# Optimization experiments

Measured on AMD Instinct MI355X. Metric: run time of the kernel, lower is better.

The kernel has to match this reference:

```python
import jax, jax.numpy as jnp
import numpy as np

N = 100000
E = 500000
F_IN = 128
HID = 64
HEADS = 4
OUT = 32
NEG_SLOPE = 0.2


def _glorot(key, shape):
    fan_in, fan_out = shape[0], shape[1]
    lim = jnp.sqrt(6.0 / (fan_in + fan_out))
    return jax.random.uniform(key, shape, jnp.float32, -lim, lim)


def setup_inputs() -> dict:
    key = jax.random.key(0)
    ks = jax.random.split(key, 20)
    x = jax.random.normal(ks[0], (N, F_IN), jnp.float32)
    edge_index = jax.random.randint(ks[1], (2, E), 0, N, jnp.int64)
    edge_attr = jax.random.uniform(ks[2], (E, 1), jnp.float32)
    d1 = HEADS * HID
    params = {
        # conv1: F_IN -> HEADS x HID
        "Wl1": _glorot(ks[3], (F_IN, d1)), "bl1": jnp.zeros((d1,), jnp.float32),
        "Wr1": _glorot(ks[4], (F_IN, d1)), "br1": jnp.zeros((d1,), jnp.float32),
        "We1": _glorot(ks[5], (1, d1)),
        "att1": _glorot(ks[6], (HEADS, HID)),
        "b1": jnp.zeros((d1,), jnp.float32),
        "Wl2": _glorot(ks[7], (d1, OUT)), "bl2": jnp.zeros((OUT,), jnp.float32),
        "Wr2": _glorot(ks[8], (d1, OUT)), "br2": jnp.zeros((OUT,), jnp.float32),
        "We2": _glorot(ks[9], (1, OUT)),
        "att2": _glorot(ks[10], (1, OUT)),
        "b2": jnp.zeros((OUT,), jnp.float32),
    }
    return {"x": x, "edge_index": edge_index, "edge_attr": edge_attr, **params}


def gatv2_conv(x, src, dst, edge_attr, Wl, bl, Wr, br, We, att, bias, heads, out_ch):
    """PyG GATv2Conv (add_self_loops=False, concat=True, share_weights=False)."""
    n = x.shape[0]
    xl = (x @ Wl + bl).reshape(n, heads, out_ch)          # source transform
    xr = (x @ Wr + br).reshape(n, heads, out_ch)          # target transform
    e = (edge_attr @ We).reshape(-1, heads, out_ch)       # [E, H, C]
    m = jax.nn.leaky_relu(xl[src] + xr[dst] + e, NEG_SLOPE)  # [E, H, C]
    alpha = jnp.einsum('ehc,hc->eh', m, att)              # [E, H]
    # softmax over edges sharing the same destination node
    amax = jax.ops.segment_max(alpha, dst, num_segments=n)
    ealpha = jnp.exp(alpha - amax[dst])
    denom = jax.ops.segment_sum(ealpha, dst, num_segments=n)
    alpha = ealpha / (denom[dst] + 1e-16)
    out = jax.ops.segment_sum(xl[src] * alpha[:, :, None], dst, num_segments=n)
    return out.reshape(n, heads * out_ch) + bias


def reference(x, edge_index, edge_attr, Wl1, bl1, Wr1, br1, We1, att1, b1,
              Wl2, bl2, Wr2, br2, We2, att2, b2):
    src, dst = edge_index[0], edge_index[1]
    h = gatv2_conv(x, src, dst, edge_attr, Wl1, bl1, Wr1, br1, We1, att1, b1, HEADS, HID)
    h = jax.nn.relu(h)  # dropout is identity at inference
    out = gatv2_conv(h, src, dst, edge_attr, Wl2, bl2, Wr2, br2, We2, att2, b2, 1, OUT)
    return out
```

## Files before the change

kernel.cpp:

```cpp
#include <hip/hip_runtime.h>
#include <cstddef>
#include <cstdint>

#define F_IN 128
#define D1   256
#define HEADS 4
#define HID   64
#define OUT_C 32
#define NEG   0.2f

typedef unsigned short ushort_t;
typedef __attribute__((ext_vector_type(8))) short short8;
typedef __attribute__((ext_vector_type(4))) float f32x4;
typedef __attribute__((ext_vector_type(4))) unsigned short ushort4v;

__device__ __forceinline__ float bu2f(ushort_t u) {
  return __uint_as_float(((unsigned)u) << 16);
}
__device__ __forceinline__ ushort_t f2bu(float f) {
  unsigned u = __float_as_uint(f);
  return (ushort_t)((u + 0x7FFF + ((u >> 16) & 1)) >> 16);
}

__global__ void prep_b1_k(const float* __restrict__ Wl, const float* __restrict__ Wr,
                          const float* __restrict__ bl, const float* __restrict__ br,
                          ushort_t* __restrict__ Bt, float* __restrict__ biasc) {
  int i = blockIdx.x * blockDim.x + threadIdx.x;
  int nn = i >> 7, k = i & 127;
  float v = (nn < D1) ? Wl[(size_t)k * D1 + nn] : Wr[(size_t)k * D1 + (nn - D1)];
  Bt[(size_t)nn * F_IN + k] = f2bu(v);
  if (k == 0) biasc[nn] = (nn < D1) ? bl[nn] : br[nn - D1];
}

__global__ void prep_b2_k(const float* __restrict__ Wl, const float* __restrict__ Wr,
                          const float* __restrict__ bl, const float* __restrict__ br,
                          ushort_t* __restrict__ Bt, float* __restrict__ biasc) {
  int i = blockIdx.x * blockDim.x + threadIdx.x;
  int nn = i >> 8, k = i & 255;
  float v = (nn < OUT_C) ? Wl[(size_t)k * OUT_C + nn] : Wr[(size_t)k * OUT_C + (nn - OUT_C)];
  Bt[(size_t)nn * D1 + k] = f2bu(v);
  if (k == 0) biasc[nn] = (nn < OUT_C) ? bl[nn] : br[nn - OUT_C];
}

template <int WM, int WN, int BK, bool CVT>
__global__ void mfma_gemm(const void* __restrict__ Av, const ushort_t* __restrict__ Bt,
                          const float* __restrict__ biasc, ushort_t* __restrict__ C,
                          int M, int N, int K) {
  constexpr int BM = WM * 64, BN = WN * 64;
  constexpr int LD = BK + 8;
  constexpr int CPR = BK / 8;
  __shared__ ushort_t As[BM][LD];
  __shared__ ushort_t Bs[BN][LD];
  const int tid = threadIdx.x;
  const int wave = tid >> 6, lane = tid & 63;
  const int wm = wave % WM, wn = wave / WM;
  const int quad = lane >> 4, l16 = lane & 15;
  const int m0 = blockIdx.x * BM, n0 = blockIdx.y * BN;
  const int nth = WM * WN * 64;
  f32x4 acc[4][4] = {};
  for (int k0 = 0; k0 < K; k0 += BK) {
    for (int i = tid; i < BM * CPR; i += nth) {
      int r = i / CPR, ch = i % CPR;
      int gr = m0 + r;
      if (CVT) {
        const float* A32 = (const float*)Av;
        f32x4 v0 = {}, v1 = {};
        if (gr < M) {
          const float* p = A32 + (size_t)gr * K + k0 + ch * 8;
          v0 = *(const f32x4*)p;
          v1 = *(const f32x4*)(p + 4);
        }
        short8 o;
        o[0] = (short)f2bu(v0[0]); o[1] = (short)f2bu(v0[1]);
        o[2] = (short)f2bu(v0[2]); o[3] = (short)f2bu(v0[3]);
        o[4] = (short)f2bu(v1[0]); o[5] = (short)f2bu(v1[1]);
        o[6] = (short)f2bu(v1[2]); o[7] = (short)f2bu(v1[3]);
        *(short8*)(&As[r][ch * 8]) = o;
      } else {
        const ushort_t* A16 = (const ushort_t*)Av;
        short8 v = {};
        if (gr < M) v = *(const short8*)(A16 + (size_t)gr * K + k0 + ch * 8);
        *(short8*)(&As[r][ch * 8]) = v;
      }
    }
    for (int i = tid; i < BN * CPR; i += nth) {
      int r = i / CPR, ch = i % CPR;
      short8 v = {};
      if (n0 + r < N) v = *(const short8*)(Bt + (size_t)(n0 + r) * K + k0 + ch * 8);
      *(short8*)(&Bs[r][ch * 8]) = v;
    }
    __syncthreads();
#pragma unroll
    for (int ks = 0; ks < BK; ks += 32) {
      short8 af[4], bfr[4];
#pragma unroll
      for (int mi = 0; mi < 4; ++mi)
        af[mi] = *(const short8*)(&As[wm * 64 + mi * 16 + l16][ks + quad * 8]);
#pragma unroll
      for (int ni = 0; ni < 4; ++ni)
        bfr[ni] = *(const short8*)(&Bs[wn * 64 + ni * 16 + l16][ks + quad * 8]);
#pragma unroll
      for (int mi = 0; mi < 4; ++mi)
#pragma unroll
        for (int ni = 0; ni < 4; ++ni)
          acc[mi][ni] = __builtin_amdgcn_mfma_f32_16x16x32_bf16(af[mi], bfr[ni],
                                                                acc[mi][ni], 0, 0, 0);
    }
    __syncthreads();
  }
#pragma unroll
  for (int mi = 0; mi < 4; ++mi) {
#pragma unroll
    for (int r = 0; r < 4; ++r) {
      int grow = m0 + wm * 64 + mi * 16 + quad * 4 + r;
      if (grow >= M) continue;
#pragma unroll
      for (int ni = 0; ni < 4; ++ni) {
        int gcol = n0 + wn * 64 + ni * 16 + l16;
        C[(size_t)grow * N + gcol] = f2bu(acc[mi][ni][r] + biasc[gcol]);
      }
    }
  }
}

__global__ void hist_k(const int* __restrict__ dst, int* __restrict__ deg, int e) {
  int i = blockIdx.x * blockDim.x + threadIdx.x;
  if (i < e) atomicAdd(&deg[dst[i]], 1);
}

__global__ void scan_block_k(const int* __restrict__ deg, int* __restrict__ row_ptr,
                             int* __restrict__ bsum, int n) {
  __shared__ int s[1024];
  int i = blockIdx.x * 1024 + threadIdx.x;
  int v = (i < n) ? deg[i] : 0;
  s[threadIdx.x] = v;
  __syncthreads();
  for (int off = 1; off < 1024; off <<= 1) {
    int t = (threadIdx.x >= off) ? s[threadIdx.x - off] : 0;
    __syncthreads();
    s[threadIdx.x] += t;
    __syncthreads();
  }
  if (i < n) row_ptr[i + 1] = s[threadIdx.x];
  if (threadIdx.x == 1023) bsum[blockIdx.x] = s[1023];
}

__global__ void scan_bsum_k(int* __restrict__ bsum, int nb) {
  __shared__ int s[128];
  int v = (threadIdx.x < nb) ? bsum[threadIdx.x] : 0;
  s[threadIdx.x] = v;
  __syncthreads();
  for (int off = 1; off < 128; off <<= 1) {
    int t = (threadIdx.x >= off) ? s[threadIdx.x - off] : 0;
    __syncthreads();
    s[threadIdx.x] += t;
    __syncthreads();
  }
  if (threadIdx.x < nb) bsum[threadIdx.x] = s[threadIdx.x] - v;
}

__global__ void add_off_k(int* __restrict__ row_ptr, const int* __restrict__ bsum, int n) {
  int i = blockIdx.x * blockDim.x + threadIdx.x;
  if (i == 0) row_ptr[0] = 0;
  if (i < n) row_ptr[i + 1] += bsum[i >> 10];
}

__global__ void copy_cursor_k(const int* __restrict__ row_ptr, int* __restrict__ cursor, int n) {
  int i = blockIdx.x * blockDim.x + threadIdx.x;
  if (i < n) cursor[i] = row_ptr[i];
}

__global__ void fill_k(const int* __restrict__ src, const int* __restrict__ dst,
                       const float* __restrict__ eattr, int* __restrict__ cursor,
                       int2* __restrict__ csr, int e) {
  int i = blockIdx.x * blockDim.x + threadIdx.x;
  if (i >= e) return;
  int p = atomicAdd(&cursor[dst[i]], 1);
  csr[p] = make_int2(src[i], __float_as_int(eattr[i]));
}

__global__ void gat1_k(const int* __restrict__ row_ptr, const int2* __restrict__ csr,
                       const ushort_t* __restrict__ C1,
                       const float* __restrict__ We, const float* __restrict__ att,
                       const float* __restrict__ bias, ushort_t* __restrict__ h1, int n) {
  int node = (int)(((size_t)blockIdx.x * blockDim.x + threadIdx.x) >> 6);
  int lane = threadIdx.x & 63;
  if (node >= n) return;
  int cb = lane * 4;
  ushort4v xr4 = *(const ushort4v*)(C1 + (size_t)node * 512 + 256 + cb);
  float xrr[4], Wev[4], attv[4], acc[4] = {0.f, 0.f, 0.f, 0.f};
  float esum = 0.f;
#pragma unroll
  for (int j = 0; j < 4; ++j) {
    xrr[j] = bu2f(xr4[j]);
    Wev[j] = We[cb + j];
    attv[j] = att[cb + j];
  }
  int p = row_ptr[node], p1 = row_ptr[node + 1];
  for (; p + 4 <= p1; p += 4) {
    int2 ee[4];
#pragma unroll
    for (int u = 0; u < 4; ++u) ee[u] = csr[p + u];
    ushort4v xl4[4];
#pragma unroll
    for (int u = 0; u < 4; ++u)
      xl4[u] = *(const ushort4v*)(C1 + (size_t)ee[u].x * 512 + cb);
    float xv[4][4], v[4];
#pragma unroll
    for (int u = 0; u < 4; ++u) {
      float wgt = __int_as_float(ee[u].y);
      v[u] = 0.f;
#pragma unroll
      for (int j = 0; j < 4; ++j) {
        xv[u][j] = bu2f(xl4[u][j]);
        float m = xv[u][j] + xrr[j] + wgt * Wev[j];
        m = m > 0.f ? m : NEG * m;
        v[u] += m * attv[j];
      }
    }
#pragma unroll
    for (int u = 0; u < 4; ++u) {
      v[u] += __shfl_xor(v[u], 1, 64);
      v[u] += __shfl_xor(v[u], 2, 64);
      v[u] += __shfl_xor(v[u], 4, 64);
      v[u] += __shfl_xor(v[u], 8, 64);
    }
#pragma unroll
    for (int u = 0; u < 4; ++u) {
      float eh = __expf(v[u]);
      esum += eh;
#pragma unroll
      for (int j = 0; j < 4; ++j) acc[j] += eh * xv[u][j];
    }
  }
  for (; p < p1; ++p) {
    int2 ed = csr[p];
    float wgt = __int_as_float(ed.y);
    ushort4v xl4 = *(const ushort4v*)(C1 + (size_t)ed.x * 512 + cb);
    float xv[4], v = 0.f;
#pragma unroll
    for (int j = 0; j < 4; ++j) {
      xv[j] = bu2f(xl4[j]);
      float m = xv[j] + xrr[j] + wgt * Wev[j];
      m = m > 0.f ? m : NEG * m;
      v += m * attv[j];
    }
    v += __shfl_xor(v, 1, 64);
    v += __shfl_xor(v, 2, 64);
    v += __shfl_xor(v, 4, 64);
    v += __shfl_xor(v, 8, 64);
    float eh = __expf(v);
    esum += eh;
#pragma unroll
    for (int j = 0; j < 4; ++j) acc[j] += eh * xv[j];
  }
  float inv = 1.f / (esum + 1e-16f);
  ushort4v o;
#pragma unroll
  for (int j = 0; j < 4; ++j) {
    float t = acc[j] * inv + bias[cb + j];
    o[j] = f2bu(t > 0.f ? t : 0.f);
  }
  *(ushort4v*)(h1 + (size_t)node * D1 + cb) = o;
}

__global__ void gat2_k(const int* __restrict__ row_ptr, const int2* __restrict__ csr,
                       const ushort_t* __restrict__ C2,
                       const float* __restrict__ We, const float* __restrict__ att,
                       const float* __restrict__ bias, float* __restrict__ out, int n) {
  size_t t = (size_t)blockIdx.x * blockDim.x + threadIdx.x;
  int node = (int)(t >> 3);
  int g = (int)(t & 7);
  if (node >= n) return;
  int cb = g * 4;
  ushort4v xr4 = *(const ushort4v*)(C2 + (size_t)node * 64 + 32 + cb);
  float xrr[4], Wev[4], attv[4], acc[4] = {0.f, 0.f, 0.f, 0.f};
  float esum = 0.f;
#pragma unroll
  for (int j = 0; j < 4; ++j) {
    xrr[j] = bu2f(xr4[j]);
    Wev[j] = We[cb + j];
    attv[j] = att[cb + j];
  }
  int p = row_ptr[node], p1 = row_ptr[node + 1];
  for (; p + 4 <= p1; p += 4) {
    int2 ee[4];
#pragma unroll
    for (int u = 0; u < 4; ++u) ee[u] = csr[p + u];
    ushort4v xl4[4];
#pragma unroll
    for (int u = 0; u < 4; ++u)
      xl4[u] = *(const ushort4v*)(C2 + (size_t)ee[u].x * 64 + cb);
    float xv[4][4], v[4];
#pragma unroll
    for (int u = 0; u < 4; ++u) {
      float wgt = __int_as_float(ee[u].y);
      v[u] = 0.f;
#pragma unroll
      for (int j = 0; j < 4; ++j) {
        xv[u][j] = bu2f(xl4[u][j]);
        float m = xv[u][j] + xrr[j] + wgt * Wev[j];
        m = m > 0.f ? m : NEG * m;
        v[u] += m * attv[j];
      }
    }
#pragma unroll
    for (int u = 0; u < 4; ++u) {
      v[u] += __shfl_xor(v[u], 1, 64);
      v[u] += __shfl_xor(v[u], 2, 64);
      v[u] += __shfl_xor(v[u], 4, 64);
    }
#pragma unroll
    for (int u = 0; u < 4; ++u) {
      float eh = __expf(v[u]);
      esum += eh;
#pragma unroll
      for (int j = 0; j < 4; ++j) acc[j] += eh * xv[u][j];
    }
  }
  for (; p < p1; ++p) {
    int2 ed = csr[p];
    float wgt = __int_as_float(ed.y);
    ushort4v xl4 = *(const ushort4v*)(C2 + (size_t)ed.x * 64 + cb);
    float xv[4], v = 0.f;
#pragma unroll
    for (int j = 0; j < 4; ++j) {
      xv[j] = bu2f(xl4[j]);
      float m = xv[j] + xrr[j] + wgt * Wev[j];
      m = m > 0.f ? m : NEG * m;
      v += m * attv[j];
    }
    v += __shfl_xor(v, 1, 64);
    v += __shfl_xor(v, 2, 64);
    v += __shfl_xor(v, 4, 64);
    float eh = __expf(v);
    esum += eh;
#pragma unroll
    for (int j = 0; j < 4; ++j) acc[j] += eh * xv[j];
  }
  float inv = 1.f / (esum + 1e-16f);
  f32x4 ov;
#pragma unroll
  for (int j = 0; j < 4; ++j) ov[j] = acc[j] * inv + bias[cb + j];
  *(f32x4*)(out + (size_t)node * OUT_C + cb) = ov;
}

extern "C" void kernel_launch(void* const* d_in, const int* in_sizes, int n_in,
                              void* d_out, int out_size, void* d_ws, size_t ws_size,
                              hipStream_t stream) {
  const float* x     = (const float*)d_in[0];
  const int*   eidx  = (const int*)d_in[1];
  const float* eattr = (const float*)d_in[2];
  const float* Wl1 = (const float*)d_in[3];
  const float* bl1 = (const float*)d_in[4];
  const float* Wr1 = (const float*)d_in[5];
  const float* br1 = (const float*)d_in[6];
  const float* We1 = (const float*)d_in[7];
  const float* att1 = (const float*)d_in[8];
  const float* b1  = (const float*)d_in[9];
  const float* Wl2 = (const float*)d_in[10];
  const float* bl2 = (const float*)d_in[11];
  const float* Wr2 = (const float*)d_in[12];
  const float* br2 = (const float*)d_in[13];
  const float* We2 = (const float*)d_in[14];
  const float* att2 = (const float*)d_in[15];
  const float* b2  = (const float*)d_in[16];

  const int n = in_sizes[0] / F_IN;
  const int e = in_sizes[2];
  const int* src = eidx;
  const int* dst = eidx + e;
  float* out = (float*)d_out;

  char* w = (char*)d_ws;
  ushort_t* C1   = (ushort_t*)w;  w += (size_t)n * 512 * 2;
  ushort_t* h1b  = (ushort_t*)w;  w += (size_t)n * D1 * 2;
  ushort_t* C2   = (ushort_t*)w;  w += (size_t)n * 64 * 2;
  ushort_t* Bt1  = (ushort_t*)w;  w += 512 * F_IN * 2;
  ushort_t* Bt2  = (ushort_t*)w;  w += 64 * D1 * 2;
  float* bias1c  = (float*)w;     w += 512 * 4;
  float* bias2c  = (float*)w;     w += 64 * 4;
  int2*  csr     = (int2*)w;      w += (size_t)e * 8;
  int*   row_ptr = (int*)w;       w += ((size_t)n + 1) * 4;
  int*   cursor  = (int*)w;       w += (size_t)n * 4;
  int*   bsum    = (int*)w;       w += 512;
  int*   deg = cursor;

  dim3 blk(256);
  const int nb = (n + 1023) / 1024;

  prep_b1_k<<<(512 * 128) / 256, blk, 0, stream>>>(Wl1, Wr1, bl1, br1, Bt1, bias1c);
  prep_b2_k<<<(64 * 256) / 256, blk, 0, stream>>>(Wl2, Wr2, bl2, br2, Bt2, bias2c);

  hipMemsetAsync(deg, 0, (size_t)n * sizeof(int), stream);
  hist_k<<<(e + 255) / 256, blk, 0, stream>>>(dst, deg, e);
  scan_block_k<<<nb, 1024, 0, stream>>>(deg, row_ptr, bsum, n);
  scan_bsum_k<<<1, 128, 0, stream>>>(bsum, nb);
  add_off_k<<<(n + 255) / 256, blk, 0, stream>>>(row_ptr, bsum, n);
  copy_cursor_k<<<(n + 255) / 256, blk, 0, stream>>>(row_ptr, cursor, n);
  fill_k<<<(e + 255) / 256, blk, 0, stream>>>(src, dst, eattr, cursor, csr, e);

  mfma_gemm<2, 2, 64, true><<<dim3((n + 127) / 128, 4), blk, 0, stream>>>(
      x, Bt1, bias1c, C1, n, 512, F_IN);
  gat1_k<<<(n + 3) / 4, blk, 0, stream>>>(row_ptr, csr, C1, We1, att1, b1, h1b, n);

  mfma_gemm<2, 1, 64, false><<<dim3((n + 127) / 128, 1), dim3(128), 0, stream>>>(
      h1b, Bt2, bias2c, C2, n, 64, D1);
  gat2_k<<<((size_t)n * 8 + 255) / 256, blk, 0, stream>>>(row_ptr, csr, C2,
                                                          We2, att2, b2, out, n);
}
```

Baseline: 349.6 us.

## Merge prep kernels, fuse cursor copy, swap GEMM grid order, widen gat2 to full wave

```diff
diff --git a/kernel.cpp b/kernel.cpp
--- a/kernel.cpp
+++ b/kernel.cpp
@@ -22,24 +22,26 @@
   return (ushort_t)((u + 0x7FFF + ((u >> 16) & 1)) >> 16);
 }
 
-__global__ void prep_b1_k(const float* __restrict__ Wl, const float* __restrict__ Wr,
-                          const float* __restrict__ bl, const float* __restrict__ br,
-                          ushort_t* __restrict__ Bt, float* __restrict__ biasc) {
-  int i = blockIdx.x * blockDim.x + threadIdx.x;
-  int nn = i >> 7, k = i & 127;
-  float v = (nn < D1) ? Wl[(size_t)k * D1 + nn] : Wr[(size_t)k * D1 + (nn - D1)];
-  Bt[(size_t)nn * F_IN + k] = f2bu(v);
-  if (k == 0) biasc[nn] = (nn < D1) ? bl[nn] : br[nn - D1];
-}
-
-__global__ void prep_b2_k(const float* __restrict__ Wl, const float* __restrict__ Wr,
-                          const float* __restrict__ bl, const float* __restrict__ br,
-                          ushort_t* __restrict__ Bt, float* __restrict__ biasc) {
-  int i = blockIdx.x * blockDim.x + threadIdx.x;
-  int nn = i >> 8, k = i & 255;
-  float v = (nn < OUT_C) ? Wl[(size_t)k * OUT_C + nn] : Wr[(size_t)k * OUT_C + (nn - OUT_C)];
-  Bt[(size_t)nn * D1 + k] = f2bu(v);
-  if (k == 0) biasc[nn] = (nn < OUT_C) ? bl[nn] : br[nn - OUT_C];
+__global__ void prep_k(const float* __restrict__ Wl1, const float* __restrict__ Wr1,
+                       const float* __restrict__ bl1, const float* __restrict__ br1,
+                       ushort_t* __restrict__ Bt1, float* __restrict__ bias1c,
+                       const float* __restrict__ Wl2, const float* __restrict__ Wr2,
+                       const float* __restrict__ bl2, const float* __restrict__ br2,
+                       ushort_t* __restrict__ Bt2, float* __restrict__ bias2c) {
+  int b = blockIdx.x;
+  if (b < 256) {
+    int i = b * 256 + threadIdx.x;
+    int nn = i >> 7, k = i & 127;
+    float v = (nn < D1) ? Wl1[(size_t)k * D1 + nn] : Wr1[(size_t)k * D1 + (nn - D1)];
+    Bt1[(size_t)nn * F_IN + k] = f2bu(v);
+    if (k == 0) bias1c[nn] = (nn < D1) ? bl1[nn] : br1[nn - D1];
+  } else {
+    int i = (b - 256) * 256 + threadIdx.x;
+    int nn = i >> 8, k = i & 255;
+    float v = (nn < OUT_C) ? Wl2[(size_t)k * OUT_C + nn] : Wr2[(size_t)k * OUT_C + (nn - OUT_C)];
+    Bt2[(size_t)nn * D1 + k] = f2bu(v);
+    if (k == 0) bias2c[nn] = (nn < OUT_C) ? bl2[nn] : br2[nn - OUT_C];
+  }
 }
 
 template <int WM, int WN, int BK, bool CVT>
@@ -55,7 +57,7 @@
   const int wave = tid >> 6, lane = tid & 63;
   const int wm = wave % WM, wn = wave / WM;
   const int quad = lane >> 4, l16 = lane & 15;
-  const int m0 = blockIdx.x * BM, n0 = blockIdx.y * BN;
+  const int m0 = blockIdx.y * BM, n0 = blockIdx.x * BN;
   const int nth = WM * WN * 64;
   f32x4 acc[4][4] = {};
   for (int k0 = 0; k0 < K; k0 += BK) {
@@ -159,15 +161,15 @@
   if (threadIdx.x < nb) bsum[threadIdx.x] = s[threadIdx.x] - v;
 }
 
-__global__ void add_off_k(int* __restrict__ row_ptr, const int* __restrict__ bsum, int n) {
+__global__ void add_off_k(int* __restrict__ row_ptr, int* __restrict__ cursor,
+                          const int* __restrict__ bsum, int n) {
   int i = blockIdx.x * blockDim.x + threadIdx.x;
-  if (i == 0) row_ptr[0] = 0;
-  if (i < n) row_ptr[i + 1] += bsum[i >> 10];
-}
-
-__global__ void copy_cursor_k(const int* __restrict__ row_ptr, int* __restrict__ cursor, int n) {
-  int i = blockIdx.x * blockDim.x + threadIdx.x;
-  if (i < n) cursor[i] = row_ptr[i];
+  if (i == 0) { row_ptr[0] = 0; cursor[0] = 0; }
+  if (i < n) {
+    int v = row_ptr[i + 1] + bsum[i >> 10];
+    row_ptr[i + 1] = v;
+    if (i + 1 < n) cursor[i + 1] = v;
+  }
 }
 
 __global__ void fill_k(const int* __restrict__ src, const int* __restrict__ dst,
@@ -197,10 +199,14 @@
     attv[j] = att[cb + j];
   }
   int p = row_ptr[node], p1 = row_ptr[node + 1];
-  for (; p + 4 <= p1; p += 4) {
+  int pl = p1 - 1;
+  for (int pb = p; pb < p1; pb += 4) {
     int2 ee[4];
 #pragma unroll
-    for (int u = 0; u < 4; ++u) ee[u] = csr[p + u];
+    for (int u = 0; u < 4; ++u) {
+      int q = pb + u;
+      ee[u] = csr[q < p1 ? q : pl];
+    }
     ushort4v xl4[4];
 #pragma unroll
     for (int u = 0; u < 4; ++u)
@@ -214,7 +220,7 @@
       for (int j = 0; j < 4; ++j) {
         xv[u][j] = bu2f(xl4[u][j]);
         float m = xv[u][j] + xrr[j] + wgt * Wev[j];
-        m = m > 0.f ? m : NEG * m;
+        m = fmaxf(m, NEG * m);
         v[u] += m * attv[j];
       }
     }
@@ -227,32 +233,11 @@
     }
 #pragma unroll
     for (int u = 0; u < 4; ++u) {
-      float eh = __expf(v[u]);
+      float eh = (pb + u < p1) ? __expf(v[u]) : 0.f;
       esum += eh;
 #pragma unroll
       for (int j = 0; j < 4; ++j) acc[j] += eh * xv[u][j];
     }
-  }
-  for (; p < p1; ++p) {
-    int2 ed = csr[p];
-    float wgt = __int_as_float(ed.y);
-    ushort4v xl4 = *(const ushort4v*)(C1 + (size_t)ed.x * 512 + cb);
-    float xv[4], v = 0.f;
-#pragma unroll
-    for (int j = 0; j < 4; ++j) {
-      xv[j] = bu2f(xl4[j]);
-      float m = xv[j] + xrr[j] + wgt * Wev[j];
-      m = m > 0.f ? m : NEG * m;
-      v += m * attv[j];
-    }
-    v += __shfl_xor(v, 1, 64);
-    v += __shfl_xor(v, 2, 64);
-    v += __shfl_xor(v, 4, 64);
-    v += __shfl_xor(v, 8, 64);
-    float eh = __expf(v);
-    esum += eh;
-#pragma unroll
-    for (int j = 0; j < 4; ++j) acc[j] += eh * xv[j];
   }
   float inv = 1.f / (esum + 1e-16f);
   ushort4v o;
@@ -268,11 +253,11 @@
                        const ushort_t* __restrict__ C2,
                        const float* __restrict__ We, const float* __restrict__ att,
                        const float* __restrict__ bias, float* __restrict__ out, int n) {
-  size_t t = (size_t)blockIdx.x * blockDim.x + threadIdx.x;
-  int node = (int)(t >> 3);
-  int g = (int)(t & 7);
+  int node = (int)(((size_t)blockIdx.x * blockDim.x + threadIdx.x) >> 6);
+  int lane = threadIdx.x & 63;
   if (node >= n) return;
-  int cb = g * 4;
+  int g = lane >> 3;
+  int cb = (lane & 7) * 4;
   ushort4v xr4 = *(const ushort4v*)(C2 + (size_t)node * 64 + 32 + cb);
   float xrr[4], Wev[4], attv[4], acc[4] = {0.f, 0.f, 0.f, 0.f};
   float esum = 0.f;
@@ -283,43 +268,10 @@
     attv[j] = att[cb + j];
   }
   int p = row_ptr[node], p1 = row_ptr[node + 1];
-  for (; p + 4 <= p1; p += 4) {
-    int2 ee[4];
-#pragma unroll
-    for (int u = 0; u < 4; ++u) ee[u] = csr[p + u];
-    ushort4v xl4[4];
-#pragma unroll
-    for (int u = 0; u < 4; ++u)
-      xl4[u] = *(const ushort4v*)(C2 + (size_t)ee[u].x * 64 + cb);
-    float xv[4][4], v[4];
-#pragma unroll
-    for (int u = 0; u < 4; ++u) {
-      float wgt = __int_as_float(ee[u].y);
-      v[u] = 0.f;
-#pragma unroll
-      for (int j = 0; j < 4; ++j) {
-        xv[u][j] = bu2f(xl4[u][j]);
-        float m = xv[u][j] + xrr[j] + wgt * Wev[j];
-        m = m > 0.f ? m : NEG * m;
-        v[u] += m * attv[j];
-      }
-    }
-#pragma unroll
-    for (int u = 0; u < 4; ++u) {
-      v[u] += __shfl_xor(v[u], 1, 64);
-      v[u] += __shfl_xor(v[u], 2, 64);
-      v[u] += __shfl_xor(v[u], 4, 64);
-    }
-#pragma unroll
-    for (int u = 0; u < 4; ++u) {
-      float eh = __expf(v[u]);
-      esum += eh;
-#pragma unroll
-      for (int j = 0; j < 4; ++j) acc[j] += eh * xv[u][j];
-    }
-  }
-  for (; p < p1; ++p) {
-    int2 ed = csr[p];
+  int pl = p1 - 1;
+  for (int pb = p; pb < p1; pb += 8) {
+    int q = pb + g;
+    int2 ed = csr[q < p1 ? q : pl];
     float wgt = __int_as_float(ed.y);
     ushort4v xl4 = *(const ushort4v*)(C2 + (size_t)ed.x * 64 + cb);
     float xv[4], v = 0.f;
@@ -327,22 +279,33 @@
     for (int j = 0; j < 4; ++j) {
       xv[j] = bu2f(xl4[j]);
       float m = xv[j] + xrr[j] + wgt * Wev[j];
-      m = m > 0.f ? m : NEG * m;
+      m = fmaxf(m, NEG * m);
       v += m * attv[j];
     }
     v += __shfl_xor(v, 1, 64);
     v += __shfl_xor(v, 2, 64);
     v += __shfl_xor(v, 4, 64);
-    float eh = __expf(v);
+    float eh = (q < p1) ? __expf(v) : 0.f;
     esum += eh;
 #pragma unroll
     for (int j = 0; j < 4; ++j) acc[j] += eh * xv[j];
   }
-  float inv = 1.f / (esum + 1e-16f);
-  f32x4 ov;
-#pragma unroll
-  for (int j = 0; j < 4; ++j) ov[j] = acc[j] * inv + bias[cb + j];
-  *(f32x4*)(out + (size_t)node * OUT_C + cb) = ov;
+  esum += __shfl_xor(esum, 8, 64);
+  esum += __shfl_xor(esum, 16, 64);
+  esum += __shfl_xor(esum, 32, 64);
+#pragma unroll
+  for (int j = 0; j < 4; ++j) {
+    acc[j] += __shfl_xor(acc[j], 8, 64);
+    acc[j] += __shfl_xor(acc[j], 16, 64);
+    acc[j] += __shfl_xor(acc[j], 32, 64);
+  }
+  if (lane < 8) {
+    float inv = 1.f / (esum + 1e-16f);
+    f32x4 ov;
+#pragma unroll
+    for (int j = 0; j < 4; ++j) ov[j] = acc[j] * inv + bias[cb + j];
+    *(f32x4*)(out + (size_t)node * OUT_C + cb) = ov;
+  }
 }
 
 extern "C" void kernel_launch(void* const* d_in, const int* in_sizes, int n_in,
@@ -389,23 +352,21 @@
   dim3 blk(256);
   const int nb = (n + 1023) / 1024;
 
-  prep_b1_k<<<(512 * 128) / 256, blk, 0, stream>>>(Wl1, Wr1, bl1, br1, Bt1, bias1c);
-  prep_b2_k<<<(64 * 256) / 256, blk, 0, stream>>>(Wl2, Wr2, bl2, br2, Bt2, bias2c);
+  prep_k<<<320, blk, 0, stream>>>(Wl1, Wr1, bl1, br1, Bt1, bias1c,
+                                  Wl2, Wr2, bl2, br2, Bt2, bias2c);
 
   hipMemsetAsync(deg, 0, (size_t)n * sizeof(int), stream);
   hist_k<<<(e + 255) / 256, blk, 0, stream>>>(dst, deg, e);
   scan_block_k<<<nb, 1024, 0, stream>>>(deg, row_ptr, bsum, n);
   scan_bsum_k<<<1, 128, 0, stream>>>(bsum, nb);
-  add_off_k<<<(n + 255) / 256, blk, 0, stream>>>(row_ptr, bsum, n);
-  copy_cursor_k<<<(n + 255) / 256, blk, 0, stream>>>(row_ptr, cursor, n);
+  add_off_k<<<(n + 255) / 256, blk, 0, stream>>>(row_ptr, cursor, bsum, n);
   fill_k<<<(e + 255) / 256, blk, 0, stream>>>(src, dst, eattr, cursor, csr, e);
 
-  mfma_gemm<2, 2, 64, true><<<dim3((n + 127) / 128, 4), blk, 0, stream>>>(
+  mfma_gemm<2, 2, 64, true><<<dim3(4, (n + 127) / 128), blk, 0, stream>>>(
       x, Bt1, bias1c, C1, n, 512, F_IN);
   gat1_k<<<(n + 3) / 4, blk, 0, stream>>>(row_ptr, csr, C1, We1, att1, b1, h1b, n);
 
-  mfma_gemm<2, 1, 64, false><<<dim3((n + 127) / 128, 1), dim3(128), 0, stream>>>(
+  mfma_gemm<2, 1, 64, false><<<dim3(1, (n + 127) / 128), dim3(128), 0, stream>>>(
       h1b, Bt2, bias2c, C2, n, 64, D1);
-  gat2_k<<<((size_t)n * 8 + 255) / 256, blk, 0, stream>>>(row_ptr, csr, C2,
-                                                          We2, att2, b2, out, n);
-}
+  gat2_k<<<(n + 3) / 4, blk, 0, stream>>>(row_ptr, csr, C2, We2, att2, b2, out, n);
+}
```

Result: slower. 368.6 us (+5.4%).
